# Kernel tuning notes

Measured on AMD Instinct MI355X. Metric: run time of the kernel, lower is better.

The kernel has to match this reference:

```python
import jax, jax.numpy as jnp
import numpy as np

N_NODES = 50000
N_EDGES = 1600000
HID = 128
N_LAYERS = 3
N_GRAPHS = 64
LN_EPS = 1e-5


def setup_inputs() -> dict:
    key = jax.random.key(0)
    ks = jax.random.split(key, 8)
    x = jax.random.normal(ks[0], (N_NODES, HID), dtype=jnp.float32)
    edge_index = jax.random.randint(ks[1], (2, N_EDGES), 0, N_NODES)
    batch = jnp.sort(jax.random.randint(ks[2], (N_NODES,), 0, N_GRAPHS))
    s = 1.0 / np.sqrt(HID)
    Wn = jax.random.normal(ks[3], (N_LAYERS, HID, HID), dtype=jnp.float32) * s   # lin_l (neighbors)
    bn = jnp.zeros((N_LAYERS, HID), dtype=jnp.float32)                           # lin_l bias
    Wr = jax.random.normal(ks[4], (N_LAYERS, HID, HID), dtype=jnp.float32) * s   # lin_r (root), no bias
    gamma = jnp.ones((N_LAYERS, HID), dtype=jnp.float32)
    beta = jnp.zeros((N_LAYERS, HID), dtype=jnp.float32)
    return {"x": x, "Wn": Wn, "bn": bn, "Wr": Wr, "gamma": gamma, "beta": beta,
            "edge_index": edge_index, "batch": batch}


def _layer_norm(h, g, b):
    mu = jnp.mean(h, axis=-1, keepdims=True)
    var = jnp.mean((h - mu) ** 2, axis=-1, keepdims=True)
    return (h - mu) * jax.lax.rsqrt(var + LN_EPS) * g + b


def reference(x, Wn, bn, Wr, gamma, beta, edge_index, batch):
    src, dst = edge_index[0], edge_index[1]
    N = x.shape[0]
    # in-degree for mean aggregation (clamped to avoid div-by-zero for isolated nodes)
    deg = jax.ops.segment_sum(jnp.ones((src.shape[0],), x.dtype), dst, num_segments=N)
    inv_deg = 1.0 / jnp.maximum(deg, 1.0)
    for l in range(N_LAYERS):
        # SAGEConv: lin_l(mean_neighbor) + lin_r(x)
        agg = jax.ops.segment_sum(x[src], dst, num_segments=N) * inv_deg[:, None]
        h = agg @ Wn[l] + bn[l] + x @ Wr[l]
        h = _layer_norm(h, gamma[l], beta[l])
        x = jax.nn.relu(h)  # dropout is identity in eval mode
    node_emb = x
    cnt = jax.ops.segment_sum(jnp.ones((N,), x.dtype), batch, num_segments=N_GRAPHS)
    graph_emb = jax.ops.segment_sum(node_emb, batch, num_segments=N_GRAPHS) / jnp.maximum(cnt, 1.0)[:, None]
    return graph_emb, node_emb
```

## Files before the change

### kernel.cpp

```cpp
#include <hip/hip_runtime.h>

#define N_NODES 50000
#define N_EDGES 1600000
#define HID     128
#define N_GRAPHS 64

#define HB 256
#define EPB (N_EDGES / HB)
#define HWORDS 12500
#define NPP 12500
#define CWPP (NPP / 4)

#define WS_DEG   0u
#define WS_BSUM  50000u
#define WS_BOFF  50256u
#define WS_OFFS  50512u
#define WS_INVD  100512u
#define WS_CSR   150512u
#define WS_XB_B  1750512u
#define WS_XB_A  4950512u
#define WS_WP    8150512u
#define WS_END   8199664u

typedef __attribute__((ext_vector_type(8))) short short8;
typedef __attribute__((ext_vector_type(4))) float floatx4;

__device__ __forceinline__ float bf_lo(unsigned u) { return __uint_as_float(u << 16); }
__device__ __forceinline__ float bf_hi(unsigned u) { return __uint_as_float(u & 0xffff0000u); }
__device__ __forceinline__ unsigned bf_rn(float f) {
    unsigned u = __float_as_uint(f);
    unsigned r = ((u >> 16) & 1u) + 0x7fffu;
    return (u + r) >> 16;
}
__device__ __forceinline__ unsigned bf_pack(float lo, float hi) {
    return bf_rn(lo) | (bf_rn(hi) << 16);
}

__global__ __launch_bounds__(256) void k_prep(const float4* __restrict__ x, uint2* __restrict__ o,
                                              const float* __restrict__ Wn, const float* __restrict__ Wr,
                                              uint4* __restrict__ wp) {
    if (blockIdx.x < 6250) {
        int i = blockIdx.x * 256 + threadIdx.x;
        float4 v = x[i];
        uint2 r;
        r.x = bf_pack(v.x, v.y);
        r.y = bf_pack(v.z, v.w);
        o[i] = r;
    } else {
        int idx = (blockIdx.x - 6250) * 256 + threadIdx.x;
        int layer = idx >> 12;
        int rem = idx & 4095;
        int kb = rem >> 9;
        int n = (rem >> 2) & 127;
        int quad = rem & 3;
        float v[8];
#pragma unroll
        for (int j = 0; j < 8; j++) {
            int k = kb * 32 + quad * 8 + j;
            v[j] = (k < 128) ? Wn[layer * 16384 + k * 128 + n]
                             : Wr[layer * 16384 + (k - 128) * 128 + n];
        }
        uint4 r;
        r.x = bf_pack(v[0], v[1]);
        r.y = bf_pack(v[2], v[3]);
        r.z = bf_pack(v[4], v[5]);
        r.w = bf_pack(v[6], v[7]);
        wp[idx] = r;
    }
}


__global__ __launch_bounds__(256) void k_hist(const int* __restrict__ ei, unsigned* __restrict__ hist) {
    __shared__ unsigned sh[HWORDS];
    for (int i = threadIdx.x; i < HWORDS; i += 256) sh[i] = 0;
    __syncthreads();
    const int e0 = blockIdx.x * EPB;
    for (int i = threadIdx.x; i < EPB; i += 256) {
        int d = __builtin_nontemporal_load(ei + N_EDGES + e0 + i);
        atomicAdd(&sh[d >> 2], 1u << ((d & 3) << 3));
    }
    __syncthreads();
    unsigned* hb = hist + (size_t)blockIdx.x * HWORDS;
    for (int i = threadIdx.x; i < HWORDS; i += 256) hb[i] = sh[i];
}

__global__ __launch_bounds__(256) void k_scanb(unsigned* __restrict__ hist, int* __restrict__ deg,
                                               int* __restrict__ bsum) {
    int w = blockIdx.x * 256 + threadIdx.x;
    int mysum = 0;
    if (w < HWORDS) {
        unsigned run = 0;
#pragma unroll 8
        for (int b = 0; b < HB; ++b) {
            unsigned u = hist[(size_t)b * HWORDS + w];
            hist[(size_t)b * HWORDS + w] = run;
            run += u;
        }
#pragma unroll
        for (int k = 0; k < 4; ++k) {
            int d = (int)((run >> (k << 3)) & 0xffu);
            deg[4 * w + k] = d;
            mysum += d;
        }
    }
    __shared__ int s[256];
    s[threadIdx.x] = mysum;
    __syncthreads();
    for (int d = 128; d > 0; d >>= 1) {
        if (threadIdx.x < d) s[threadIdx.x] += s[threadIdx.x + d];
        __syncthreads();
    }
    if (threadIdx.x == 0) bsum[blockIdx.x] = s[0];
}

__global__ __launch_bounds__(256) void k_scanblocks(const int* __restrict__ bsum, int* __restrict__ boff, int nb) {
    __shared__ int s[256];
    int t = threadIdx.x;
    int v = (t < nb) ? bsum[t] : 0;
    s[t] = v;
    __syncthreads();
    for (int d = 1; d < 256; d <<= 1) {
        int add = (t >= d) ? s[t - d] : 0;
        __syncthreads();
        s[t] += add;
        __syncthreads();
    }
    if (t < nb) boff[t] = s[t] - v;
}

__global__ __launch_bounds__(256) void k_offsets(const int* __restrict__ deg, const int* __restrict__ boff,
                                                 int* __restrict__ offs, float* __restrict__ invdeg) {
    __shared__ int s[256];
    int b = blockIdx.x, t = threadIdx.x;
    int n0 = (b * 256 + t) * 4;
    int d[4] = {0, 0, 0, 0};
#pragma unroll
    for (int k = 0; k < 4; ++k)
        if (n0 + k < N_NODES) d[k] = deg[n0 + k];
    int v = d[0] + d[1] + d[2] + d[3];
    s[t] = v;
    __syncthreads();
    for (int dd = 1; dd < 256; dd <<= 1) {
        int add = (t >= dd) ? s[t - dd] : 0;
        __syncthreads();
        s[t] += add;
        __syncthreads();
    }
    int base = boff[b] + s[t] - v;
#pragma unroll
    for (int k = 0; k < 4; ++k) {
        if (n0 + k < N_NODES) {
            offs[n0 + k] = base;
            invdeg[n0 + k] = 1.0f / fmaxf((float)d[k], 1.0f);
            base += d[k];
        }
    }
}

__global__ __launch_bounds__(256) void k_fill(const int* __restrict__ ei, const int* __restrict__ offs,
                                              const unsigned* __restrict__ hist, int* __restrict__ csr) {
    __shared__ unsigned scur[CWPP];
    const int s8 = blockIdx.x & 7;
    const int pass = s8 >> 1;
    const int b = ((blockIdx.x >> 3) << 1) | (s8 & 1);
    const int nbase = pass * NPP;
    const unsigned* hb = hist + (size_t)b * HWORDS + pass * CWPP;
    for (int i = threadIdx.x; i < CWPP; i += 256) scur[i] = hb[i];
    __syncthreads();
    const int e0 = b * EPB;
    for (int i = threadIdx.x; i < EPB; i += 256) {
        int d = __builtin_nontemporal_load(ei + N_EDGES + e0 + i);
        unsigned rd = (unsigned)(d - nbase);
        if (rd < (unsigned)NPP) {
            int s = ei[e0 + i];
            int sh = (rd & 3) << 3;
            unsigned old = atomicAdd(&scur[rd >> 2], 1u << sh);
            unsigned rel = (old >> sh) & 0xffu;
            csr[offs[d] + (int)rel] = s * 16;
        }
    }
}


__global__ __launch_bounds__(256) void k_layer16(
        const uint4* __restrict__ xq, const int* __restrict__ csr,
        const int* __restrict__ offs, const int* __restrict__ deg,
        const float* __restrict__ invdeg, const uint4* __restrict__ wp,
        const float* __restrict__ bn, const float* __restrict__ gam,
        const float* __restrict__ bet, float* __restrict__ xout,
        unsigned* __restrict__ b16out, int write_f32) {
    __shared__ float H[16 * 132];
    uint4* A = (uint4*)H;

    const int t = threadIdx.x;
    const int wv = t >> 6;
    const int lane = t & 63;
    const int slot = lane >> 4;
    const int m = lane & 15;
    const int n0 = blockIdx.x * 16;
    const uint4* xm = xq + m;

    for (int i = 0; i < 4; ++i) {
        int node = __builtin_amdgcn_readfirstlane(n0 + wv * 4 + i);
        const int beg = offs[node];
        const int dn = deg[node];
        float a0 = 0.f, a1 = 0.f, a2 = 0.f, a3 = 0.f, a4 = 0.f, a5 = 0.f, a6 = 0.f, a7 = 0.f;
        int j = slot;
        for (; j + 32 <= dn; j += 32) {
            int s0 = csr[beg + j];
            int s1 = csr[beg + j + 4];
            int s2 = csr[beg + j + 8];
            int s3 = csr[beg + j + 12];
            int s4 = csr[beg + j + 16];
            int s5 = csr[beg + j + 20];
            int s6 = csr[beg + j + 24];
            int s7 = csr[beg + j + 28];
            uint4 u0 = xm[s0], u1 = xm[s1], u2 = xm[s2], u3 = xm[s3];
            uint4 u4 = xm[s4], u5 = xm[s5], u6 = xm[s6], u7 = xm[s7];
            a0 += ((bf_lo(u0.x) + bf_lo(u1.x)) + (bf_lo(u2.x) + bf_lo(u3.x))) + ((bf_lo(u4.x) + bf_lo(u5.x)) + (bf_lo(u6.x) + bf_lo(u7.x)));
            a1 += ((bf_hi(u0.x) + bf_hi(u1.x)) + (bf_hi(u2.x) + bf_hi(u3.x))) + ((bf_hi(u4.x) + bf_hi(u5.x)) + (bf_hi(u6.x) + bf_hi(u7.x)));
            a2 += ((bf_lo(u0.y) + bf_lo(u1.y)) + (bf_lo(u2.y) + bf_lo(u3.y))) + ((bf_lo(u4.y) + bf_lo(u5.y)) + (bf_lo(u6.y) + bf_lo(u7.y)));
            a3 += ((bf_hi(u0.y) + bf_hi(u1.y)) + (bf_hi(u2.y) + bf_hi(u3.y))) + ((bf_hi(u4.y) + bf_hi(u5.y)) + (bf_hi(u6.y) + bf_hi(u7.y)));
            a4 += ((bf_lo(u0.z) + bf_lo(u1.z)) + (bf_lo(u2.z) + bf_lo(u3.z))) + ((bf_lo(u4.z) + bf_lo(u5.z)) + (bf_lo(u6.z) + bf_lo(u7.z)));
            a5 += ((bf_hi(u0.z) + bf_hi(u1.z)) + (bf_hi(u2.z) + bf_hi(u3.z))) + ((bf_hi(u4.z) + bf_hi(u5.z)) + (bf_hi(u6.z) + bf_hi(u7.z)));
            a6 += ((bf_lo(u0.w) + bf_lo(u1.w)) + (bf_lo(u2.w) + bf_lo(u3.w))) + ((bf_lo(u4.w) + bf_lo(u5.w)) + (bf_lo(u6.w) + bf_lo(u7.w)));
            a7 += ((bf_hi(u0.w) + bf_hi(u1.w)) + (bf_hi(u2.w) + bf_hi(u3.w))) + ((bf_hi(u4.w) + bf_hi(u5.w)) + (bf_hi(u6.w) + bf_hi(u7.w)));
        }
        for (; j + 16 <= dn; j += 16) {
            int s0 = csr[beg + j];
            int s1 = csr[beg + j + 4];
            int s2 = csr[beg + j + 8];
            int s3 = csr[beg + j + 12];
            uint4 u0 = xm[s0], u1 = xm[s1], u2 = xm[s2], u3 = xm[s3];
            a0 += (bf_lo(u0.x) + bf_lo(u1.x)) + (bf_lo(u2.x) + bf_lo(u3.x));
            a1 += (bf_hi(u0.x) + bf_hi(u1.x)) + (bf_hi(u2.x) + bf_hi(u3.x));
            a2 += (bf_lo(u0.y) + bf_lo(u1.y)) + (bf_lo(u2.y) + bf_lo(u3.y));
            a3 += (bf_hi(u0.y) + bf_hi(u1.y)) + (bf_hi(u2.y) + bf_hi(u3.y));
            a4 += (bf_lo(u0.z) + bf_lo(u1.z)) + (bf_lo(u2.z) + bf_lo(u3.z));
            a5 += (bf_hi(u0.z) + bf_hi(u1.z)) + (bf_hi(u2.z) + bf_hi(u3.z));
            a6 += (bf_lo(u0.w) + bf_lo(u1.w)) + (bf_lo(u2.w) + bf_lo(u3.w));
            a7 += (bf_hi(u0.w) + bf_hi(u1.w)) + (bf_hi(u2.w) + bf_hi(u3.w));
        }
        for (; j < dn; j += 4) {
            uint4 u0 = xm[csr[beg + j]];
            a0 += bf_lo(u0.x); a1 += bf_hi(u0.x);
            a2 += bf_lo(u0.y); a3 += bf_hi(u0.y);
            a4 += bf_lo(u0.z); a5 += bf_hi(u0.z);
            a6 += bf_lo(u0.w); a7 += bf_hi(u0.w);
        }
#pragma unroll
        for (int msk = 16; msk < 64; msk <<= 1) {
            a0 += __shfl_xor(a0, msk); a1 += __shfl_xor(a1, msk);
            a2 += __shfl_xor(a2, msk); a3 += __shfl_xor(a3, msk);
            a4 += __shfl_xor(a4, msk); a5 += __shfl_xor(a5, msk);
            a6 += __shfl_xor(a6, msk); a7 += __shfl_xor(a7, msk);
        }
        if (slot == 0) {
            float id = invdeg[node];
            uint4 r;
            r.x = bf_pack(a0 * id, a1 * id);
            r.y = bf_pack(a2 * id, a3 * id);
            r.z = bf_pack(a4 * id, a5 * id);
            r.w = bf_pack(a6 * id, a7 * id);
            A[(wv * 4 + i) * 17 + m] = r;
        }
    }
    __syncthreads();

    const int quad = lane >> 4;
    const int nl = lane & 15;
    const int nb = wv * 32;
    floatx4 acc0 = {0.f, 0.f, 0.f, 0.f}, acc1 = acc0;
#pragma unroll
    for (int kb = 0; kb < 8; ++kb) {
        uint4 av = (kb < 4) ? A[nl * 17 + kb * 4 + quad]
                            : xq[(n0 + nl) * 16 + (kb - 4) * 4 + quad];
        uint4 b0 = wp[(kb * 128 + nb + nl) * 4 + quad];
        uint4 b1 = wp[(kb * 128 + nb + 16 + nl) * 4 + quad];
        short8 as = *(short8*)&av;
        short8 b0s = *(short8*)&b0, b1s = *(short8*)&b1;
        acc0 = __builtin_amdgcn_mfma_f32_16x16x32_bf16(as, b0s, acc0, 0, 0, 0);
        acc1 = __builtin_amdgcn_mfma_f32_16x16x32_bf16(as, b1s, acc1, 0, 0, 0);
    }
    __syncthreads();

    float bn0 = bn[nb + nl];
    float bn1 = bn[nb + 16 + nl];
#pragma unroll
    for (int reg = 0; reg < 4; ++reg) {
        int rr = quad * 4 + reg;
        H[rr * 132 + nb + nl] = acc0[reg] + bn0;
        H[rr * 132 + nb + 16 + nl] = acc1[reg] + bn1;
    }
    __syncthreads();

    const int row = t >> 4;
    const int sub = t & 15;
    const float* hr = &H[row * 132 + sub * 8];
    float v[8];
    float s = 0.f, s2 = 0.f;
#pragma unroll
    for (int i = 0; i < 8; i++) {
        v[i] = hr[i];
        s += v[i];
        s2 += v[i] * v[i];
    }
#pragma unroll
    for (int msk = 1; msk < 16; msk <<= 1) {
        s += __shfl_xor(s, msk);
        s2 += __shfl_xor(s2, msk);
    }
    float mean = s * (1.f / 128.f);
    float var = s2 * (1.f / 128.f) - mean * mean;
    float rstd = rsqrtf(var + 1e-5f);
    const int gr = n0 + row;
    const int cb = sub * 8;
    float o[8];
#pragma unroll
    for (int i = 0; i < 8; i++)
        o[i] = fmaxf((v[i] - mean) * rstd * gam[cb + i] + bet[cb + i], 0.f);
    if (write_f32) {
        *(float4*)&xout[(size_t)gr * HID + cb] = *(float4*)&o[0];
        *(float4*)&xout[(size_t)gr * HID + cb + 4] = *(float4*)&o[4];
    }
    unsigned p[4];
#pragma unroll
    for (int i = 0; i < 4; i++) p[i] = bf_pack(o[2 * i], o[2 * i + 1]);
    *(uint4*)&b16out[(size_t)gr * 64 + (cb >> 1)] = *(uint4*)&p[0];
}


__global__ __launch_bounds__(1024) void k_pool_seg(const unsigned* __restrict__ xb,
                                                   const int* __restrict__ batch,
                                                   float* __restrict__ out) {
    const int g = blockIdx.x;
    __shared__ int s_beg, s_end;
    if (threadIdx.x == 0) {
        int lo = 0, hi = N_NODES;
        while (lo < hi) { int mid = (lo + hi) >> 1; if (batch[mid] < g) lo = mid + 1; else hi = mid; }
        s_beg = lo;
        lo = 0; hi = N_NODES;
        while (lo < hi) { int mid = (lo + hi) >> 1; if (batch[mid] < g + 1) lo = mid + 1; else hi = mid; }
        s_end = lo;
    }
    __syncthreads();
    const int beg = s_beg, end = s_end;
    const int w = threadIdx.x & 63;
    const int q = threadIdx.x >> 6;
    float ax = 0.f, ay = 0.f;
    for (int r = beg + q; r < end; r += 16) {
        unsigned u = xb[(size_t)r * 64 + w];
        ax += bf_lo(u);
        ay += bf_hi(u);
    }
    __shared__ float sx[16][64], sy[16][64];
    sx[q][w] = ax;
    sy[q][w] = ay;
    __syncthreads();
    if (q == 0) {
        float tx = 0.f, ty = 0.f;
#pragma unroll
        for (int i = 0; i < 16; i++) { tx += sx[i][w]; ty += sy[i][w]; }
        float inv = 1.f / fmaxf((float)(end - beg), 1.f);
        float2 r;
        r.x = tx * inv;
        r.y = ty * inv;
        *(float2*)&out[(g << 7) + w * 2] = r;
    }
}

extern "C" void kernel_launch(void* const* d_in, const int* in_sizes, int n_in,
                              void* d_out, int out_size, void* d_ws, size_t ws_size,
                              hipStream_t stream) {
    const float* x0 = (const float*)d_in[0];
    const float* Wn = (const float*)d_in[1];
    const float* bn = (const float*)d_in[2];
    const float* Wr = (const float*)d_in[3];
    const float* gam = (const float*)d_in[4];
    const float* bet = (const float*)d_in[5];
    const int* ei = (const int*)d_in[6];
    const int* batch = (const int*)d_in[7];

    float* out = (float*)d_out;
    float* node_out = out + N_GRAPHS * HID;

    unsigned* ws = (unsigned*)d_ws;
    int* deg = (int*)(ws + WS_DEG);
    int* bsum = (int*)(ws + WS_BSUM);
    int* boff = (int*)(ws + WS_BOFF);
    int* offs = (int*)(ws + WS_OFFS);
    float* invdeg = (float*)(ws + WS_INVD);
    int* csr = (int*)(ws + WS_CSR);
    unsigned* hist = ws + WS_XB_B;
    unsigned* xa = ws + WS_XB_A;
    unsigned* xbb = ws + WS_XB_B;
    uint4* wp = (uint4*)(ws + WS_WP);

    k_prep<<<6298, 256, 0, stream>>>((const float4*)x0, (uint2*)xa, Wn, Wr, wp);
    k_hist<<<HB, 256, 0, stream>>>(ei, hist);
    k_scanb<<<49, 256, 0, stream>>>(hist, deg, bsum);
    k_scanblocks<<<1, 256, 0, stream>>>(bsum, boff, 49);
    k_offsets<<<49, 256, 0, stream>>>(deg, boff, offs, invdeg);
    k_fill<<<HB * 4, 256, 0, stream>>>(ei, offs, hist, csr);

    const int lb = N_NODES / 16;

    for (int l = 0; l < 3; ++l) {
        const unsigned* xin = (l & 1) ? xbb : xa;
        unsigned* xout16 = (l & 1) ? xa : xbb;
        k_layer16<<<lb, 256, 0, stream>>>((const uint4*)xin, csr, offs, deg, invdeg,
                                          wp + (size_t)l * 4096, bn + (size_t)l * HID,
                                          gam + (size_t)l * HID, bet + (size_t)l * HID,
                                          node_out, xout16, l == 2 ? 1 : 0);
    }

    k_pool_seg<<<N_GRAPHS, 1024, 0, stream>>>(xbb, batch, out);
}
```

Measured before the change: 466.0 us.

## Use 1024-thread layer blocks with one wave per node for gather

```diff
diff --git a/kernel.cpp b/kernel.cpp
--- a/kernel.cpp
+++ b/kernel.cpp
@@ -182,15 +182,15 @@
 }
 
 
-__global__ __launch_bounds__(256) void k_layer16(
+__global__ __launch_bounds__(1024) void k_layer1k(
         const uint4* __restrict__ xq, const int* __restrict__ csr,
         const int* __restrict__ offs, const int* __restrict__ deg,
         const float* __restrict__ invdeg, const uint4* __restrict__ wp,
         const float* __restrict__ bn, const float* __restrict__ gam,
         const float* __restrict__ bet, float* __restrict__ xout,
         unsigned* __restrict__ b16out, int write_f32) {
+    __shared__ uint4 A[16 * 17];
     __shared__ float H[16 * 132];
-    uint4* A = (uint4*)H;
 
     const int t = threadIdx.x;
     const int wv = t >> 6;
@@ -200,8 +200,8 @@
     const int n0 = blockIdx.x * 16;
     const uint4* xm = xq + m;
 
-    for (int i = 0; i < 4; ++i) {
-        int node = __builtin_amdgcn_readfirstlane(n0 + wv * 4 + i);
+    {
+        const int node = n0 + wv;
         const int beg = offs[node];
         const int dn = deg[node];
         float a0 = 0.f, a1 = 0.f, a2 = 0.f, a3 = 0.f, a4 = 0.f, a5 = 0.f, a6 = 0.f, a7 = 0.f;
@@ -262,71 +262,56 @@
             r.y = bf_pack(a2 * id, a3 * id);
             r.z = bf_pack(a4 * id, a5 * id);
             r.w = bf_pack(a6 * id, a7 * id);
-            A[(wv * 4 + i) * 17 + m] = r;
-        }
-    }
-    __syncthreads();
-
-    const int quad = lane >> 4;
-    const int nl = lane & 15;
-    const int nb = wv * 32;
-    floatx4 acc0 = {0.f, 0.f, 0.f, 0.f}, acc1 = acc0;
-#pragma unroll
-    for (int kb = 0; kb < 8; ++kb) {
-        uint4 av = (kb < 4) ? A[nl * 17 + kb * 4 + quad]
-                            : xq[(n0 + nl) * 16 + (kb - 4) * 4 + quad];
-        uint4 b0 = wp[(kb * 128 + nb + nl) * 4 + quad];
-        uint4 b1 = wp[(kb * 128 + nb + 16 + nl) * 4 + quad];
-        short8 as = *(short8*)&av;
-        short8 b0s = *(short8*)&b0, b1s = *(short8*)&b1;
-        acc0 = __builtin_amdgcn_mfma_f32_16x16x32_bf16(as, b0s, acc0, 0, 0, 0);
-        acc1 = __builtin_amdgcn_mfma_f32_16x16x32_bf16(as, b1s, acc1, 0, 0, 0);
-    }
-    __syncthreads();
-
-    float bn0 = bn[nb + nl];
-    float bn1 = bn[nb + 16 + nl];
-#pragma unroll
-    for (int reg = 0; reg < 4; ++reg) {
-        int rr = quad * 4 + reg;
-        H[rr * 132 + nb + nl] = acc0[reg] + bn0;
-        H[rr * 132 + nb + 16 + nl] = acc1[reg] + bn1;
-    }
-    __syncthreads();
-
-    const int row = t >> 4;
-    const int sub = t & 15;
-    const float* hr = &H[row * 132 + sub * 8];
-    float v[8];
-    float s = 0.f, s2 = 0.f;
-#pragma unroll
-    for (int i = 0; i < 8; i++) {
-        v[i] = hr[i];
-        s += v[i];
-        s2 += v[i] * v[i];
-    }
-#pragma unroll
-    for (int msk = 1; msk < 16; msk <<= 1) {
-        s += __shfl_xor(s, msk);
-        s2 += __shfl_xor(s2, msk);
-    }
-    float mean = s * (1.f / 128.f);
-    float var = s2 * (1.f / 128.f) - mean * mean;
-    float rstd = rsqrtf(var + 1e-5f);
-    const int gr = n0 + row;
-    const int cb = sub * 8;
-    float o[8];
-#pragma unroll
-    for (int i = 0; i < 8; i++)
-        o[i] = fmaxf((v[i] - mean) * rstd * gam[cb + i] + bet[cb + i], 0.f);
-    if (write_f32) {
-        *(float4*)&xout[(size_t)gr * HID + cb] = *(float4*)&o[0];
-        *(float4*)&xout[(size_t)gr * HID + cb + 4] = *(float4*)&o[4];
-    }
-    unsigned p[4];
-#pragma unroll
-    for (int i = 0; i < 4; i++) p[i] = bf_pack(o[2 * i], o[2 * i + 1]);
-    *(uint4*)&b16out[(size_t)gr * 64 + (cb >> 1)] = *(uint4*)&p[0];
+            A[wv * 17 + m] = r;
+        }
+    }
+    __syncthreads();
+
+    if (wv < 8) {
+        const int quad = lane >> 4;
+        const int nl = lane & 15;
+        const int nt = wv;
+        floatx4 acc = {0.f, 0.f, 0.f, 0.f};
+#pragma unroll
+        for (int kb = 0; kb < 8; ++kb) {
+            uint4 av = (kb < 4) ? A[nl * 17 + kb * 4 + quad]
+                                : xq[(n0 + nl) * 16 + (kb - 4) * 4 + quad];
+            uint4 bv = wp[(kb * 128 + nt * 16 + nl) * 4 + quad];
+            short8 as = *(short8*)&av;
+            short8 bs = *(short8*)&bv;
+            acc = __builtin_amdgcn_mfma_f32_16x16x32_bf16(as, bs, acc, 0, 0, 0);
+        }
+        float bnv = bn[nt * 16 + nl];
+#pragma unroll
+        for (int reg = 0; reg < 4; ++reg)
+            H[(quad * 4 + reg) * 132 + nt * 16 + nl] = acc[reg] + bnv;
+    }
+    __syncthreads();
+
+    {
+        float2 hv = *(const float2*)&H[wv * 132 + lane * 2];
+        float s = hv.x + hv.y;
+        float s2 = hv.x * hv.x + hv.y * hv.y;
+#pragma unroll
+        for (int msk = 1; msk < 64; msk <<= 1) {
+            s += __shfl_xor(s, msk);
+            s2 += __shfl_xor(s2, msk);
+        }
+        float mean = s * (1.f / 128.f);
+        float var = s2 * (1.f / 128.f) - mean * mean;
+        float rstd = rsqrtf(var + 1e-5f);
+        const int gr = n0 + wv;
+        const int c = lane * 2;
+        float o0 = fmaxf((hv.x - mean) * rstd * gam[c] + bet[c], 0.f);
+        float o1 = fmaxf((hv.y - mean) * rstd * gam[c + 1] + bet[c + 1], 0.f);
+        if (write_f32) {
+            float2 w2;
+            w2.x = o0;
+            w2.y = o1;
+            *(float2*)&xout[(size_t)gr * HID + c] = w2;
+        }
+        b16out[(size_t)gr * 64 + lane] = bf_pack(o0, o1);
+    }
 }
 
 
@@ -408,10 +393,10 @@
     for (int l = 0; l < 3; ++l) {
         const unsigned* xin = (l & 1) ? xbb : xa;
         unsigned* xout16 = (l & 1) ? xa : xbb;
-        k_layer16<<<lb, 256, 0, stream>>>((const uint4*)xin, csr, offs, deg, invdeg,
-                                          wp + (size_t)l * 4096, bn + (size_t)l * HID,
-                                          gam + (size_t)l * HID, bet + (size_t)l * HID,
-                                          node_out, xout16, l == 2 ? 1 : 0);
+        k_layer1k<<<lb, 1024, 0, stream>>>((const uint4*)xin, csr, offs, deg, invdeg,
+                                           wp + (size_t)l * 4096, bn + (size_t)l * HID,
+                                           gam + (size_t)l * HID, bet + (size_t)l * HID,
+                                           node_out, xout16, l == 2 ? 1 : 0);
     }
 
     k_pool_seg<<<N_GRAPHS, 1024, 0, stream>>>(xbb, batch, out);
```

Result: slower. 562.8 us (+20.8%).
